# Optimization experiments

Measured on AMD Instinct MI355X. Metric: run time of the kernel, lower is better.

The kernel has to match this reference:

```python
import jax, jax.numpy as jnp
import numpy as np

B, N, IN_DIM, SLOT_DIM, NUM_SLOTS, NUM_ITERS = 64, 4096, 256, 256, 8, 3
LN_EPS = 1e-5


def _ln(x, g, b):
    m = jnp.mean(x, axis=-1, keepdims=True)
    v = jnp.mean(jnp.square(x - m), axis=-1, keepdims=True)
    return (x - m) * jax.lax.rsqrt(v + LN_EPS) * g + b


def setup_inputs() -> dict:
    key = jax.random.key(0)
    ks = jax.random.split(key, 16)
    D, I = SLOT_DIM, IN_DIM
    s = 0.02
    return {
        "inputs": jax.random.normal(ks[0], (B, N, I), jnp.float32),
        "slots_noise": jax.random.normal(ks[1], (B, NUM_SLOTS, D), jnp.float32),
        "slots_mu": jax.random.normal(ks[2], (1, 1, D), jnp.float32),
        "slots_log_sigma": jnp.zeros((1, 1, D), jnp.float32),
        "ln_in_g": jnp.ones((I,), jnp.float32), "ln_in_b": jnp.zeros((I,), jnp.float32),
        "ln_s_g": jnp.ones((D,), jnp.float32), "ln_s_b": jnp.zeros((D,), jnp.float32),
        "ln_m_g": jnp.ones((D,), jnp.float32), "ln_m_b": jnp.zeros((D,), jnp.float32),
        "Wq": jax.random.normal(ks[3], (D, D), jnp.float32) * s,
        "Wk": jax.random.normal(ks[4], (I, D), jnp.float32) * s,
        "Wv": jax.random.normal(ks[5], (I, D), jnp.float32) * s,
        "gru_w_ih": jax.random.normal(ks[6], (3 * D, D), jnp.float32) * s,
        "gru_w_hh": jax.random.normal(ks[7], (3 * D, D), jnp.float32) * s,
        "gru_b_ih": jnp.zeros((3 * D,), jnp.float32),
        "gru_b_hh": jnp.zeros((3 * D,), jnp.float32),
        "mlp_w1": jax.random.normal(ks[8], (D, 4 * D), jnp.float32) * s,
        "mlp_b1": jnp.zeros((4 * D,), jnp.float32),
        "mlp_w2": jax.random.normal(ks[9], (4 * D, D), jnp.float32) * s,
        "mlp_b2": jnp.zeros((D,), jnp.float32),
    }


def reference(inputs, slots_noise, slots_mu, slots_log_sigma, ln_in_g, ln_in_b,
              ln_s_g, ln_s_b, ln_m_g, ln_m_b, Wq, Wk, Wv,
              gru_w_ih, gru_w_hh, gru_b_ih, gru_b_hh,
              mlp_w1, mlp_b1, mlp_w2, mlp_b2):
    D = SLOT_DIM
    # slot init: mu + sigma * noise
    slots = slots_mu + jnp.exp(slots_log_sigma) * slots_noise  # [B, S, D]
    x = _ln(inputs, ln_in_g, ln_in_b)                          # [B, N, I]
    k = x @ Wk                                                 # [B, N, D]
    v = x @ Wv                                                 # [B, N, D]
    scale = 1.0 / jnp.sqrt(jnp.float32(D))
    attn = None
    for _ in range(NUM_ITERS):
        slots_prev = slots
        s_n = _ln(slots, ln_s_g, ln_s_b)
        q = s_n @ Wq                                           # [B, S, D]
        logits = jnp.einsum('bnd,bmd->bnm', k, q) * scale      # [B, N, S]
        attn = jax.nn.softmax(logits, axis=-1)                 # softmax over slots
        attn_nrm = attn / (jnp.sum(attn, axis=1, keepdims=True) + 1e-8)
        updates = jnp.einsum('bnm,bnd->bmd', attn_nrm, v)      # [B, S, D]
        # GRUCell (PyTorch semantics)
        gi = updates @ gru_w_ih.T + gru_b_ih                   # [B, S, 3D]
        gh = slots_prev @ gru_w_hh.T + gru_b_hh
        gi_r, gi_z, gi_n = jnp.split(gi, 3, axis=-1)
        gh_r, gh_z, gh_n = jnp.split(gh, 3, axis=-1)
        r = jax.nn.sigmoid(gi_r + gh_r)
        z = jax.nn.sigmoid(gi_z + gh_z)
        n = jnp.tanh(gi_n + r * gh_n)
        slots = (1.0 - z) * n + z * slots_prev
        # residual MLP
        h = jax.nn.relu(_ln(slots, ln_m_g, ln_m_b) @ mlp_w1 + mlp_b1)
        slots = slots + h @ mlp_w2 + mlp_b2
    return slots, jnp.transpose(attn, (0, 2, 1))
```

## Files before the change

kernel.cpp:

```cpp
#include <hip/hip_runtime.h>


typedef unsigned short u16;
typedef __attribute__((ext_vector_type(8))) short bf16x8;
typedef __attribute__((ext_vector_type(4))) float f32x4;

#define MFMA16(a, b, c) __builtin_amdgcn_mfma_f32_16x16x32_bf16((a), (b), (c), 0, 0, 0)

__device__ __forceinline__ u16 f2bf(float f) {
  union { float f; unsigned u; } v; v.f = f;
  unsigned r = (v.u + 0x7fffu + ((v.u >> 16) & 1u)) >> 16;
  return (u16)r;
}
__device__ __forceinline__ float sigm(float x) { return 1.f / (1.f + __expf(-x)); }
__device__ __forceinline__ float tanh_f(float x) { return 1.f - 2.f / (1.f + __expf(2.f * x)); }

__global__ __launch_bounds__(256) void prep_kernel(
    const float* __restrict__ Wq, const float* __restrict__ Wk, const float* __restrict__ Wv,
    const float* __restrict__ wih, const float* __restrict__ whh,
    const float* __restrict__ w1, const float* __restrict__ w2,
    u16* __restrict__ wkB, u16* __restrict__ wqT, u16* __restrict__ wvT,
    u16* __restrict__ wihB, u16* __restrict__ whhB, u16* __restrict__ w1T, u16* __restrict__ w2T) {
  const int bid = blockIdx.x;
  const int tid = threadIdx.x;
  if (bid < 160) {
    __shared__ float tile[64][65];
    const float* src; u16* dst; int R, C, t;
    if (bid < 16)      { src = Wq; dst = wqT; R = 256;  C = 256;  t = bid; }
    else if (bid < 32) { src = Wv; dst = wvT; R = 256;  C = 256;  t = bid - 16; }
    else if (bid < 96) { src = w1; dst = w1T; R = 1024; C = 256;  t = bid - 32; }
    else               { src = w2; dst = w2T; R = 256;  C = 1024; t = bid - 96; }
    const int tilesJ = C >> 6;
    const int i0 = (t / tilesJ) * 64, j0 = (t % tilesJ) * 64;
    const int c = tid & 63, r0 = tid >> 6;
#pragma unroll
    for (int rr = 0; rr < 16; rr++) {
      int row = rr * 4 + r0;
      tile[row][c] = src[(size_t)(j0 + row) * R + i0 + c];
    }
    __syncthreads();
#pragma unroll
    for (int rr = 0; rr < 16; rr++) {
      int row = rr * 4 + r0;
      dst[(size_t)(i0 + row) * C + j0 + c] = f2bf(tile[c][row]);
    }
  } else {
    int gid = (bid - 160) * 256 + tid;
    for (int i4 = gid; i4 < 114688; i4 += 64 * 256) {
      int i = i4 * 4;
      const float* s; u16* d; int off;
      if (i < 65536) { s = Wk; d = wkB; off = i; }
      else if (i < 262144) { s = wih; d = wihB; off = i - 65536; }
      else { s = whh; d = whhB; off = i - 262144; }
      float4 v = *reinterpret_cast<const float4*>(s + off);
      unsigned lo = (unsigned)f2bf(v.x) | ((unsigned)f2bf(v.y) << 16);
      unsigned hi = (unsigned)f2bf(v.z) | ((unsigned)f2bf(v.w) << 16);
      *reinterpret_cast<uint2*>(d + off) = make_uint2(lo, hi);
    }
  }
}

__device__ __forceinline__ void ln_row16(const float (*src)[264], u16 (*dst)[264],
                                         const float* __restrict__ g, const float* __restrict__ bb,
                                         int wave, int lane) {
  int row = wave;
  if (row < 8) {
    float4 v = *reinterpret_cast<const float4*>(&src[row][lane * 4]);
    float s = v.x + v.y + v.z + v.w;
    float sq = v.x * v.x + v.y * v.y + v.z * v.z + v.w * v.w;
#pragma unroll
    for (int m = 1; m < 64; m <<= 1) { s += __shfl_xor(s, m); sq += __shfl_xor(sq, m); }
    float mu = s * (1.f / 256.f);
    float var = sq * (1.f / 256.f) - mu * mu;
    float rstd = rsqrtf(fmaxf(var, 0.f) + 1e-5f);
    float4 gg = *reinterpret_cast<const float4*>(&g[lane * 4]);
    float4 bv = *reinterpret_cast<const float4*>(&bb[lane * 4]);
    unsigned lo = (unsigned)f2bf((v.x - mu) * rstd * gg.x + bv.x) |
                  ((unsigned)f2bf((v.y - mu) * rstd * gg.y + bv.y) << 16);
    unsigned hi = (unsigned)f2bf((v.z - mu) * rstd * gg.z + bv.z) |
                  ((unsigned)f2bf((v.w - mu) * rstd * gg.w + bv.w) << 16);
    *reinterpret_cast<uint2*>(&dst[row][lane * 4]) = make_uint2(lo, hi);
  } else if (row < 16) {
    *reinterpret_cast<uint2*>(&dst[row][lane * 4]) = make_uint2(0, 0);
  }
}

__global__ __launch_bounds__(1024, 4) void slot_kernel(
    float* __restrict__ slots, u16* __restrict__ qg, float* __restrict__ cd,
    const float* __restrict__ wsY, const float* __restrict__ wsS,
    const u16* __restrict__ wvT, const u16* __restrict__ wihB, const u16* __restrict__ whhB,
    const u16* __restrict__ w1T, const u16* __restrict__ w2T, const u16* __restrict__ wqT,
    const u16* __restrict__ wkB,
    const float* __restrict__ bih, const float* __restrict__ bhh,
    const float* __restrict__ b1v, const float* __restrict__ b2v,
    const float* __restrict__ g_in, const float* __restrict__ b_in,
    const float* __restrict__ g_s, const float* __restrict__ b_s,
    const float* __restrict__ g_m, const float* __restrict__ b_m,
    const float* __restrict__ s_mu, const float* __restrict__ s_ls,
    const float* __restrict__ noise,
    float* __restrict__ d_out, int do_update) {
  __shared__ alignas(16) char pool[58368];
  u16 (*h_lds)[1032] = reinterpret_cast<u16(*)[1032]>(pool);
  u16 (*u_lds)[264] = reinterpret_cast<u16(*)[264]>(pool);
  u16 (*uv_lds)[264] = reinterpret_cast<u16(*)[264]>(pool + 8448);
  u16 (*sb_lds)[264] = reinterpret_cast<u16(*)[264]>(pool + 16896);
  u16 (*m_lds)[264] = reinterpret_cast<u16(*)[264]>(pool + 33024);
  float (*ns_lds)[264] = reinterpret_cast<float(*)[264]>(pool + 41472);
  u16 (*q_lds)[264] = reinterpret_cast<u16(*)[264]>(pool + 41472);
  __shared__ float sS0[16], sS1[16], sInv[16];
  __shared__ float redq[16][4][4][2];

  const int b = blockIdx.x;
  const int tid = threadIdx.x;
  const int lane = tid & 63, wave = tid >> 6;
  const int quad = lane >> 4, col = lane & 15;
  const int i256 = tid & 255, s4 = tid >> 8;
  const f32x4 vzero = {0.f, 0.f, 0.f, 0.f};

  if (do_update) {
    if (tid < 16) {
      float S0 = 0.f, S1 = 0.f;
      if (tid < 8) {
        for (int c = 0; c < 32; c++) {
          S0 += wsS[((b * 32 + c) * 8 + tid) * 2 + 0];
          S1 += wsS[((b * 32 + c) * 8 + tid) * 2 + 1];
        }
      }
      sS0[tid] = S0; sS1[tid] = S1; sInv[tid] = 1.f / (S0 + 1e-8f);
    }
#pragma unroll
    for (int r = 0; r < 4; r++) {
      int s = s4 + r * 4;
      sb_lds[s][i256] = (s < 8) ? f2bf(slots[(size_t)(b * 8 + s) * 256 + i256]) : (u16)0;
    }
    __syncthreads();
    {
      float gv = g_in[i256], bv = b_in[i256];
#pragma unroll
      for (int r = 0; r < 4; r++) {
        int s = s4 + r * 4;
        if (s < 8) {
          float y = 0.f;
#pragma unroll
          for (int c = 0; c < 32; c++) y += wsY[((size_t)((b * 32 + c) * 8 + s)) * 256 + i256];
          u_lds[s][i256] = f2bf((gv * (y - sS1[s]) + bv * sS0[s]) * sInv[s]);
        } else {
          u_lds[s][i256] = 0;
        }
      }
    }
    __syncthreads();
    {
      bf16x8 af[8];
#pragma unroll
      for (int k = 0; k < 8; k++)
        af[k] = *reinterpret_cast<const bf16x8*>(&u_lds[col][k * 32 + quad * 8]);
      int ct = wave;
      f32x4 acc = vzero;
#pragma unroll
      for (int k = 0; k < 8; k++) {
        bf16x8 bf = *reinterpret_cast<const bf16x8*>(wvT + (size_t)(ct * 16 + col) * 256 + k * 32 + quad * 8);
        acc = MFMA16(af[k], bf, acc);
      }
#pragma unroll
      for (int r = 0; r < 4; r++) {
        int s = quad * 4 + r;
        uv_lds[s][ct * 16 + col] = (s < 8) ? f2bf(acc[r]) : (u16)0;
      }
    }
    __syncthreads();
    {
      bf16x8 afu[8], afs[8];
#pragma unroll
      for (int k = 0; k < 8; k++) {
        afu[k] = *reinterpret_cast<const bf16x8*>(&uv_lds[col][k * 32 + quad * 8]);
        afs[k] = *reinterpret_cast<const bf16x8*>(&sb_lds[col][k * 32 + quad * 8]);
      }
      int d = wave * 16 + col;
      f32x4 a_ir = vzero, a_iz = vzero, a_in = vzero, a_hr = vzero, a_hz = vzero, a_hn = vzero;
#pragma unroll
      for (int k = 0; k < 8; k++) {
        int ko = k * 32 + quad * 8;
        a_ir = MFMA16(afu[k], *reinterpret_cast<const bf16x8*>(wihB + (size_t)(d)*256 + ko), a_ir);
        a_iz = MFMA16(afu[k], *reinterpret_cast<const bf16x8*>(wihB + (size_t)(256 + d) * 256 + ko), a_iz);
        a_in = MFMA16(afu[k], *reinterpret_cast<const bf16x8*>(wihB + (size_t)(512 + d) * 256 + ko), a_in);
        a_hr = MFMA16(afs[k], *reinterpret_cast<const bf16x8*>(whhB + (size_t)(d)*256 + ko), a_hr);
        a_hz = MFMA16(afs[k], *reinterpret_cast<const bf16x8*>(whhB + (size_t)(256 + d) * 256 + ko), a_hz);
        a_hn = MFMA16(afs[k], *reinterpret_cast<const bf16x8*>(whhB + (size_t)(512 + d) * 256 + ko), a_hn);
      }
      float bihr = bih[d], bihz = bih[256 + d], bihn = bih[512 + d];
      float bhhr = bhh[d], bhhz = bhh[256 + d], bhhn = bhh[512 + d];
#pragma unroll
      for (int r = 0; r < 4; r++) {
        int s = quad * 4 + r;
        float rg = sigm(a_ir[r] + bihr + a_hr[r] + bhhr);
        float zg = sigm(a_iz[r] + bihz + a_hz[r] + bhhz);
        float ng = tanh_f(a_in[r] + bihn + rg * (a_hn[r] + bhhn));
        float prev = (s < 8) ? slots[(size_t)(b * 8 + s) * 256 + d] : 0.f;
        float ns = (1.f - zg) * ng + zg * prev;
        ns_lds[s][d] = (s < 8) ? ns : 0.f;
      }
    }
    __syncthreads();
    ln_row16(ns_lds, m_lds, g_m, b_m, wave, lane);
    __syncthreads();
    {
      bf16x8 af[8];
#pragma unroll
      for (int k = 0; k < 8; k++)
        af[k] = *reinterpret_cast<const bf16x8*>(&m_lds[col][k * 32 + quad * 8]);
      for (int cc = 0; cc < 4; cc++) {
        int ct = wave * 4 + cc;
        f32x4 acc = vzero;
#pragma unroll
        for (int k = 0; k < 8; k++) {
          bf16x8 bf = *reinterpret_cast<const bf16x8*>(w1T + (size_t)(ct * 16 + col) * 256 + k * 32 + quad * 8);
          acc = MFMA16(af[k], bf, acc);
        }
        float bb = b1v[ct * 16 + col];
#pragma unroll
        for (int r = 0; r < 4; r++) {
          int s = quad * 4 + r;
          float h = fmaxf(acc[r] + bb, 0.f);
          h_lds[s][ct * 16 + col] = (s < 8) ? f2bf(h) : (u16)0;
        }
      }
    }
    __syncthreads();
    {
      int ct = wave;
      f32x4 acc = vzero;
      for (int k = 0; k < 32; k++) {
        bf16x8 af = *reinterpret_cast<const bf16x8*>(&h_lds[col][k * 32 + quad * 8]);
        bf16x8 bf = *reinterpret_cast<const bf16x8*>(w2T + (size_t)(ct * 16 + col) * 1024 + k * 32 + quad * 8);
        acc = MFMA16(af, bf, acc);
      }
      int d = ct * 16 + col;
      float bb = b2v[d];
#pragma unroll
      for (int r = 0; r < 4; r++) {
        int s = quad * 4 + r;
        if (s < 8) {
          float fin = ns_lds[s][d] + acc[r] + bb;
          slots[(size_t)(b * 8 + s) * 256 + d] = fin;
          d_out[(size_t)(b * 8 + s) * 256 + d] = fin;
          ns_lds[s][d] = fin;
        }
      }
    }
    __syncthreads();
  } else {
#pragma unroll
    for (int r = 0; r < 4; r++) {
      int s = s4 + r * 4;
      float v = 0.f;
      if (s < 8) {
        v = s_mu[i256] + __expf(s_ls[i256]) * noise[(size_t)(b * 8 + s) * 256 + i256];
        slots[(size_t)(b * 8 + s) * 256 + i256] = v;
      }
      ns_lds[s][i256] = v;
    }
    __syncthreads();
  }

  ln_row16(ns_lds, m_lds, g_s, b_s, wave, lane);
  __syncthreads();
  {
    bf16x8 af[8];
#pragma unroll
    for (int k = 0; k < 8; k++)
      af[k] = *reinterpret_cast<const bf16x8*>(&m_lds[col][k * 32 + quad * 8]);
    int ct = wave;
    f32x4 acc = vzero;
#pragma unroll
    for (int k = 0; k < 8; k++) {
      bf16x8 bf = *reinterpret_cast<const bf16x8*>(wqT + (size_t)(ct * 16 + col) * 256 + k * 32 + quad * 8);
      acc = MFMA16(af[k], bf, acc);
    }
#pragma unroll
    for (int r = 0; r < 4; r++) {
      int s = quad * 4 + r;
      q_lds[s][ct * 16 + col] = (s < 8) ? f2bf(acc[r]) : (u16)0;
    }
  }
  __syncthreads();
  {
    bf16x8 af[8];
#pragma unroll
    for (int k = 0; k < 8; k++)
      af[k] = *reinterpret_cast<const bf16x8*>(&q_lds[col][k * 32 + quad * 8]);
    float cacc[4] = {0.f, 0.f, 0.f, 0.f}, dacc[4] = {0.f, 0.f, 0.f, 0.f};
    int ct = wave;
    f32x4 acc = vzero;
#pragma unroll
    for (int k = 0; k < 8; k++) {
      bf16x8 bf = *reinterpret_cast<const bf16x8*>(wkB + (size_t)(ct * 16 + col) * 256 + k * 32 + quad * 8);
      acc = MFMA16(af[k], bf, acc);
    }
    int i = ct * 16 + col;
    float gi_ = g_in[i] * 0.0625f, bi_ = b_in[i] * 0.0625f;
#pragma unroll
    for (int r = 0; r < 4; r++) {
      int s = quad * 4 + r;
      float qkv = acc[r];
      float qgv = (s < 8) ? gi_ * qkv : 0.f;
      qg[(size_t)(b * 16 + s) * 256 + i] = f2bf(qgv);
      cacc[r] -= qgv;
      dacc[r] += (s < 8) ? bi_ * qkv : 0.f;
    }
#pragma unroll
    for (int r = 0; r < 4; r++) {
#pragma unroll
      for (int m = 1; m < 16; m <<= 1) {
        cacc[r] += __shfl_xor(cacc[r], m);
        dacc[r] += __shfl_xor(dacc[r], m);
      }
    }
    if (col == 0) {
#pragma unroll
      for (int r = 0; r < 4; r++) {
        redq[wave][quad][r][0] = cacc[r];
        redq[wave][quad][r][1] = dacc[r];
      }
    }
    __syncthreads();
    if (tid < 16) {
      int qd = tid >> 2, r = tid & 3;
      float c = 0.f, dd = 0.f;
      for (int w = 0; w < 16; w++) { c += redq[w][qd][r][0]; dd += redq[w][qd][r][1]; }
      cd[(b * 16 + tid) * 2 + 0] = c;
      cd[(b * 16 + tid) * 2 + 1] = dd;
    }
  }
}

template <int PASS>
__global__ __launch_bounds__(256, 5) void attn_kernel(
    const float* __restrict__ x, u16* __restrict__ xb, float2* __restrict__ stats2,
    const u16* __restrict__ qg, const float* __restrict__ cd,
    float* __restrict__ out, float* __restrict__ wsY, float* __restrict__ wsS) {
  __shared__ alignas(16) u16 x_lds[32][280];
  __shared__ alignas(16) u16 a2s[4][16][40];
  __shared__ float2 stats_lds[32];

  const int chunk = blockIdx.x, b = blockIdx.y;
  const int tid = threadIdx.x;
  const int lane = tid & 63, wave = tid >> 6;
  const int quad = lane >> 4, col = lane & 15;

  const float2 cdv = *reinterpret_cast<const float2*>(cd + (b * 16 + col) * 2);

  f32x4 Yacc[4];
#pragma unroll
  for (int cc = 0; cc < 4; cc++) Yacc[cc] = {0.f, 0.f, 0.f, 0.f};
  float s0a = 0.f, s1a = 0.f;
  float* out_attn = out + 131072;

  for (int g = 0; g < 4; g++) {
    const int nb = chunk * 128 + g * 32;
    __syncthreads();
    if (PASS == 0) {
#pragma unroll
      for (int p = 0; p < 8; p++) {
        const int row = wave * 8 + p;
        float4 v = *reinterpret_cast<const float4*>(x + (size_t)(b * 4096 + nb + row) * 256 + lane * 4);
        unsigned lo = (unsigned)f2bf(v.x) | ((unsigned)f2bf(v.y) << 16);
        unsigned hi = (unsigned)f2bf(v.z) | ((unsigned)f2bf(v.w) << 16);
        *reinterpret_cast<uint2*>(&x_lds[row][lane * 4]) = make_uint2(lo, hi);
        *reinterpret_cast<uint2*>(xb + (size_t)(b * 4096 + nb + row) * 256 + lane * 4) = make_uint2(lo, hi);
      }
    } else {
#pragma unroll
      for (int p = 0; p < 8; p++) {
        const int row = wave * 8 + p;
        *reinterpret_cast<uint2*>(&x_lds[row][lane * 4]) =
            *reinterpret_cast<const uint2*>(xb + (size_t)(b * 4096 + nb + row) * 256 + lane * 4);
      }
      if (tid < 32) stats_lds[tid] = stats2[(size_t)b * 4096 + nb + tid];
    }
    __syncthreads();

    bf16x8 bfrag[8];
#pragma unroll
    for (int k = 0; k < 8; k++)
      bfrag[k] = *reinterpret_cast<const bf16x8*>(qg + (size_t)(b * 16 + col) * 256 + k * 32 + quad * 8);
#pragma unroll
    for (int t = 0; t < 2; t++) {
      bf16x8 af[8];
#pragma unroll
      for (int k = 0; k < 8; k++)
        af[k] = *reinterpret_cast<const bf16x8*>(&x_lds[t * 16 + col][k * 32 + quad * 8]);
      f32x4 acc = {0.f, 0.f, 0.f, 0.f};
#pragma unroll
      for (int k = 0; k < 8; k++) acc = MFMA16(af[k], bfrag[k], acc);

      float rmx[4], rmy[4];
      if (PASS == 0) {
        const short one_bf = (short)0x3F80;
        bf16x8 ones8 = {one_bf, one_bf, one_bf, one_bf, one_bf, one_bf, one_bf, one_bf};
        f32x4 accS = {0.f, 0.f, 0.f, 0.f}, accG = {0.f, 0.f, 0.f, 0.f};
#pragma unroll
        for (int k = 0; k < 8; k++) {
          accS = MFMA16(af[k], ones8, accS);
          accG = MFMA16(af[k], af[k], accG);
        }
#pragma unroll
        for (int r = 0; r < 4; r++) {
          float sq = __shfl(accG[r], (quad << 4) + quad * 4 + r);
          float mu = accS[r] * (1.f / 256.f);
          float var = sq * (1.f / 256.f) - mu * mu;
          float rstd = rsqrtf(fmaxf(var, 0.f) + 1e-5f);
          rmx[r] = rstd; rmy[r] = rstd * mu;
        }
        if (wave == 0 && col == 0) {
#pragma unroll
          for (int r = 0; r < 4; r++)
            stats2[(size_t)b * 4096 + nb + t * 16 + quad * 4 + r] = make_float2(rmx[r], rmy[r]);
        }
      } else {
#pragma unroll
        for (int r = 0; r < 4; r++) {
          float2 rm = stats_lds[t * 16 + quad * 4 + r];
          rmx[r] = rm.x; rmy[r] = rm.y;
        }
      }
      float at[4];
#pragma unroll
      for (int r = 0; r < 4; r++) {
        float lg = rmx[r] * acc[r] + rmy[r] * cdv.x + cdv.y;
        float mx = lg;
        mx = fmaxf(mx, __shfl_xor(mx, 1));
        mx = fmaxf(mx, __shfl_xor(mx, 2));
        mx = fmaxf(mx, __shfl_xor(mx, 4));
        float e = __expf(lg - mx);
        float sm = e;
        sm += __shfl_xor(sm, 1); sm += __shfl_xor(sm, 2); sm += __shfl_xor(sm, 4);
        at[r] = e / sm;
      }
      if (col < 8) {
#pragma unroll
        for (int r = 0; r < 4; r++)
          a2s[wave][col][t * 16 + quad * 4 + r] = f2bf(at[r] * rmx[r]);
        if (wave == 0) {
#pragma unroll
          for (int r = 0; r < 4; r++) {
            out_attn[(size_t)(b * 8 + col) * 4096 + nb + t * 16 + quad * 4 + r] = at[r];
            s0a += at[r];
            s1a += at[r] * rmy[r];
          }
        }
      }
    }
    {
      bf16x8 afa = *reinterpret_cast<const bf16x8*>(&a2s[wave][col][quad * 8]);
#pragma unroll
      for (int cc = 0; cc < 4; cc++) {
        const int ib = (wave * 4 + cc) * 16 + col;
        union { short s[8]; bf16x8 v; } bx;
#pragma unroll
        for (int j = 0; j < 8; j++) bx.s[j] = (short)x_lds[quad * 8 + j][ib];
        Yacc[cc] = MFMA16(afa, bx.v, Yacc[cc]);
      }
    }
  }
  if (quad < 2) {
#pragma unroll
    for (int cc = 0; cc < 4; cc++) {
      int i = (wave * 4 + cc) * 16 + col;
#pragma unroll
      for (int r = 0; r < 4; r++) {
        int s = quad * 4 + r;
        wsY[(size_t)((b * 32 + chunk) * 8 + s) * 256 + i] = Yacc[cc][r];
      }
    }
  }
  s0a += __shfl_xor(s0a, 16); s0a += __shfl_xor(s0a, 32);
  s1a += __shfl_xor(s1a, 16); s1a += __shfl_xor(s1a, 32);
  if (wave == 0 && lane < 8) {
    wsS[((b * 32 + chunk) * 8 + lane) * 2 + 0] = s0a;
    wsS[((b * 32 + chunk) * 8 + lane) * 2 + 1] = s1a;
  }
}

extern "C" void kernel_launch(void* const* d_in, const int* in_sizes, int n_in,
                              void* d_out, int out_size, void* d_ws, size_t ws_size,
                              hipStream_t stream) {
  const float* inputs = (const float*)d_in[0];
  const float* noise = (const float*)d_in[1];
  const float* s_mu = (const float*)d_in[2];
  const float* s_ls = (const float*)d_in[3];
  const float* g_in = (const float*)d_in[4];
  const float* b_in = (const float*)d_in[5];
  const float* g_s = (const float*)d_in[6];
  const float* b_s = (const float*)d_in[7];
  const float* g_m = (const float*)d_in[8];
  const float* b_m = (const float*)d_in[9];
  const float* Wq = (const float*)d_in[10];
  const float* Wk = (const float*)d_in[11];
  const float* Wv = (const float*)d_in[12];
  const float* wih = (const float*)d_in[13];
  const float* whh = (const float*)d_in[14];
  const float* bih = (const float*)d_in[15];
  const float* bhh = (const float*)d_in[16];
  const float* w1 = (const float*)d_in[17];
  const float* b1v = (const float*)d_in[18];
  const float* w2 = (const float*)d_in[19];
  const float* b2v = (const float*)d_in[20];
  float* out = (float*)d_out;

  size_t o = 0;
  auto take = [&](size_t bytes) {
    void* p = (char*)d_ws + o;
    o += (bytes + 255) & ~(size_t)255;
    return p;
  };
  float* slots = (float*)take((size_t)64 * 8 * 256 * 4);
  u16* qg = (u16*)take((size_t)64 * 16 * 256 * 2);
  float* cd = (float*)take((size_t)64 * 16 * 2 * 4);
  float* wsY = (float*)take((size_t)64 * 32 * 8 * 256 * 4);
  float* wsS = (float*)take((size_t)64 * 32 * 8 * 2 * 4);
  u16* wkB = (u16*)take((size_t)65536 * 2);
  u16* wqT = (u16*)take((size_t)65536 * 2);
  u16* wvT = (u16*)take((size_t)65536 * 2);
  u16* wihB = (u16*)take((size_t)196608 * 2);
  u16* whhB = (u16*)take((size_t)196608 * 2);
  u16* w1T = (u16*)take((size_t)262144 * 2);
  u16* w2T = (u16*)take((size_t)262144 * 2);
  u16* xb = (u16*)take((size_t)64 * 4096 * 256 * 2);
  float2* stats2 = (float2*)take((size_t)64 * 4096 * 8);

  prep_kernel<<<224, 256, 0, stream>>>(Wq, Wk, Wv, wih, whh, w1, w2,
                                       wkB, wqT, wvT, wihB, whhB, w1T, w2T);
  slot_kernel<<<64, 1024, 0, stream>>>(slots, qg, cd, wsY, wsS,
                                       wvT, wihB, whhB, w1T, w2T, wqT, wkB,
                                       bih, bhh, b1v, b2v,
                                       g_in, b_in, g_s, b_s, g_m, b_m,
                                       s_mu, s_ls, noise, out, 0);
  for (int it = 0; it < 3; it++) {
    if (it == 0)
      attn_kernel<0><<<dim3(32, 64), 256, 0, stream>>>(inputs, xb, stats2, qg, cd, out, wsY, wsS);
    else
      attn_kernel<1><<<dim3(32, 64), 256, 0, stream>>>(inputs, xb, stats2, qg, cd, out, wsY, wsS);
    slot_kernel<<<64, 1024, 0, stream>>>(slots, qg, cd, wsY, wsS,
                                         wvT, wihB, whhB, w1T, w2T, wqT, wkB,
                                         bih, bhh, b1v, b2v,
                                         g_in, b_in, g_s, b_s, g_m, b_m,
                                         s_mu, s_ls, noise, out, 1);
  }
}
```

Measured before the change: 808.2 us.

## Split input conversion into separate kernel and double-buffer attention tiles

```diff
diff --git a/kernel.cpp b/kernel.cpp
--- a/kernel.cpp
+++ b/kernel.cpp
@@ -14,6 +14,37 @@
 }
 __device__ __forceinline__ float sigm(float x) { return 1.f / (1.f + __expf(-x)); }
 __device__ __forceinline__ float tanh_f(float x) { return 1.f - 2.f / (1.f + __expf(2.f * x)); }
+
+__global__ __launch_bounds__(256, 4) void xcvt_kernel(
+    const float* __restrict__ x, u16* __restrict__ xb, float2* __restrict__ stats2) {
+  const int lane = threadIdx.x & 63;
+  const int gw = blockIdx.x * 4 + (threadIdx.x >> 6);
+#pragma unroll 1
+  for (int it = 0; it < 8; it++) {
+    float4 v[4];
+    int r[4];
+#pragma unroll
+    for (int j = 0; j < 4; j++) {
+      r[j] = (it * 4 + j) * 8192 + gw;
+      v[j] = *reinterpret_cast<const float4*>(x + (size_t)r[j] * 256 + lane * 4);
+    }
+#pragma unroll
+    for (int j = 0; j < 4; j++) {
+      float4 vv = v[j];
+      float s = vv.x + vv.y + vv.z + vv.w;
+      float sq = vv.x * vv.x + vv.y * vv.y + vv.z * vv.z + vv.w * vv.w;
+#pragma unroll
+      for (int m = 1; m < 64; m <<= 1) { s += __shfl_xor(s, m); sq += __shfl_xor(sq, m); }
+      float mu = s * (1.f / 256.f);
+      float var = sq * (1.f / 256.f) - mu * mu;
+      float rstd = rsqrtf(fmaxf(var, 0.f) + 1e-5f);
+      if (lane == 0) stats2[r[j]] = make_float2(rstd, rstd * mu);
+      unsigned lo = (unsigned)f2bf(vv.x) | ((unsigned)f2bf(vv.y) << 16);
+      unsigned hi = (unsigned)f2bf(vv.z) | ((unsigned)f2bf(vv.w) << 16);
+      *reinterpret_cast<uint2*>(xb + (size_t)r[j] * 256 + lane * 4) = make_uint2(lo, hi);
+    }
+  }
+}
 
 __global__ __launch_bounds__(256) void prep_kernel(
     const float* __restrict__ Wq, const float* __restrict__ Wk, const float* __restrict__ Wv,
@@ -334,20 +365,23 @@
   }
 }
 
-template <int PASS>
-__global__ __launch_bounds__(256, 5) void attn_kernel(
-    const float* __restrict__ x, u16* __restrict__ xb, float2* __restrict__ stats2,
+__global__ __launch_bounds__(256, 3) void attn_kernel(
+    const u16* __restrict__ xb, const float2* __restrict__ stats2,
     const u16* __restrict__ qg, const float* __restrict__ cd,
     float* __restrict__ out, float* __restrict__ wsY, float* __restrict__ wsS) {
-  __shared__ alignas(16) u16 x_lds[32][280];
+  __shared__ alignas(16) u16 x_lds[2][32][280];
   __shared__ alignas(16) u16 a2s[4][16][40];
-  __shared__ float2 stats_lds[32];
+  __shared__ float2 stats_lds[2][32];
 
   const int chunk = blockIdx.x, b = blockIdx.y;
   const int tid = threadIdx.x;
   const int lane = tid & 63, wave = tid >> 6;
   const int quad = lane >> 4, col = lane & 15;
 
+  bf16x8 bfrag[8];
+#pragma unroll
+  for (int k = 0; k < 8; k++)
+    bfrag[k] = *reinterpret_cast<const bf16x8*>(qg + (size_t)(b * 16 + col) * 256 + k * 32 + quad * 8);
   const float2 cdv = *reinterpret_cast<const float2*>(cd + (b * 16 + col) * 2);
 
   f32x4 Yacc[4];
@@ -356,78 +390,47 @@
   float s0a = 0.f, s1a = 0.f;
   float* out_attn = out + 131072;
 
+  uint2 pf[8];
+  float2 pfs;
+  {
+    const int nb0 = chunk * 128;
+#pragma unroll
+    for (int p = 0; p < 8; p++)
+      pf[p] = *reinterpret_cast<const uint2*>(xb + (size_t)(b * 4096 + nb0 + wave * 8 + p) * 256 + lane * 4);
+    if (tid < 32) pfs = stats2[(size_t)b * 4096 + nb0 + tid];
+#pragma unroll
+    for (int p = 0; p < 8; p++)
+      *reinterpret_cast<uint2*>(&x_lds[0][wave * 8 + p][lane * 4]) = pf[p];
+    if (tid < 32) stats_lds[0][tid] = pfs;
+  }
+
   for (int g = 0; g < 4; g++) {
+    const int cur = g & 1;
     const int nb = chunk * 128 + g * 32;
     __syncthreads();
-    if (PASS == 0) {
-#pragma unroll
-      for (int p = 0; p < 8; p++) {
-        const int row = wave * 8 + p;
-        float4 v = *reinterpret_cast<const float4*>(x + (size_t)(b * 4096 + nb + row) * 256 + lane * 4);
-        unsigned lo = (unsigned)f2bf(v.x) | ((unsigned)f2bf(v.y) << 16);
-        unsigned hi = (unsigned)f2bf(v.z) | ((unsigned)f2bf(v.w) << 16);
-        *reinterpret_cast<uint2*>(&x_lds[row][lane * 4]) = make_uint2(lo, hi);
-        *reinterpret_cast<uint2*>(xb + (size_t)(b * 4096 + nb + row) * 256 + lane * 4) = make_uint2(lo, hi);
-      }
-    } else {
-#pragma unroll
-      for (int p = 0; p < 8; p++) {
-        const int row = wave * 8 + p;
-        *reinterpret_cast<uint2*>(&x_lds[row][lane * 4]) =
-            *reinterpret_cast<const uint2*>(xb + (size_t)(b * 4096 + nb + row) * 256 + lane * 4);
-      }
-      if (tid < 32) stats_lds[tid] = stats2[(size_t)b * 4096 + nb + tid];
-    }
-    __syncthreads();
-
-    bf16x8 bfrag[8];
-#pragma unroll
-    for (int k = 0; k < 8; k++)
-      bfrag[k] = *reinterpret_cast<const bf16x8*>(qg + (size_t)(b * 16 + col) * 256 + k * 32 + quad * 8);
+    if (g < 3) {
+      const int nbn = nb + 32;
+#pragma unroll
+      for (int p = 0; p < 8; p++)
+        pf[p] = *reinterpret_cast<const uint2*>(xb + (size_t)(b * 4096 + nbn + wave * 8 + p) * 256 + lane * 4);
+      if (tid < 32) pfs = stats2[(size_t)b * 4096 + nbn + tid];
+    }
 #pragma unroll
     for (int t = 0; t < 2; t++) {
       bf16x8 af[8];
 #pragma unroll
       for (int k = 0; k < 8; k++)
-        af[k] = *reinterpret_cast<const bf16x8*>(&x_lds[t * 16 + col][k * 32 + quad * 8]);
+        af[k] = *reinterpret_cast<const bf16x8*>(&x_lds[cur][t * 16 + col][k * 32 + quad * 8]);
       f32x4 acc = {0.f, 0.f, 0.f, 0.f};
 #pragma unroll
       for (int k = 0; k < 8; k++) acc = MFMA16(af[k], bfrag[k], acc);
 
-      float rmx[4], rmy[4];
-      if (PASS == 0) {
-        const short one_bf = (short)0x3F80;
-        bf16x8 ones8 = {one_bf, one_bf, one_bf, one_bf, one_bf, one_bf, one_bf, one_bf};
-        f32x4 accS = {0.f, 0.f, 0.f, 0.f}, accG = {0.f, 0.f, 0.f, 0.f};
-#pragma unroll
-        for (int k = 0; k < 8; k++) {
-          accS = MFMA16(af[k], ones8, accS);
-          accG = MFMA16(af[k], af[k], accG);
-        }
-#pragma unroll
-        for (int r = 0; r < 4; r++) {
-          float sq = __shfl(accG[r], (quad << 4) + quad * 4 + r);
-          float mu = accS[r] * (1.f / 256.f);
-          float var = sq * (1.f / 256.f) - mu * mu;
-          float rstd = rsqrtf(fmaxf(var, 0.f) + 1e-5f);
-          rmx[r] = rstd; rmy[r] = rstd * mu;
-        }
-        if (wave == 0 && col == 0) {
-#pragma unroll
-          for (int r = 0; r < 4; r++)
-            stats2[(size_t)b * 4096 + nb + t * 16 + quad * 4 + r] = make_float2(rmx[r], rmy[r]);
-        }
-      } else {
-#pragma unroll
-        for (int r = 0; r < 4; r++) {
-          float2 rm = stats_lds[t * 16 + quad * 4 + r];
-          rmx[r] = rm.x; rmy[r] = rm.y;
-        }
-      }
-      float at[4];
-#pragma unroll
-      for (int r = 0; r < 4; r++) {
-        float lg = rmx[r] * acc[r] + rmy[r] * cdv.x + cdv.y;
+      float at[4], rmx[4], rmy[4];
+#pragma unroll
+      for (int r = 0; r < 4; r++) {
+        float2 rm = stats_lds[cur][t * 16 + quad * 4 + r];
+        rmx[r] = rm.x; rmy[r] = rm.y;
+        float lg = rm.x * acc[r] + rm.y * cdv.x + cdv.y;
         float mx = lg;
         mx = fmaxf(mx, __shfl_xor(mx, 1));
         mx = fmaxf(mx, __shfl_xor(mx, 2));
@@ -458,9 +461,15 @@
         const int ib = (wave * 4 + cc) * 16 + col;
         union { short s[8]; bf16x8 v; } bx;
 #pragma unroll
-        for (int j = 0; j < 8; j++) bx.s[j] = (short)x_lds[quad * 8 + j][ib];
+        for (int j = 0; j < 8; j++) bx.s[j] = (short)x_lds[cur][quad * 8 + j][ib];
         Yacc[cc] = MFMA16(afa, bx.v, Yacc[cc]);
       }
+    }
+    if (g < 3) {
+#pragma unroll
+      for (int p = 0; p < 8; p++)
+        *reinterpret_cast<uint2*>(&x_lds[cur ^ 1][wave * 8 + p][lane * 4]) = pf[p];
+      if (tid < 32) stats_lds[cur ^ 1][tid] = pfs;
     }
   }
   if (quad < 2) {
@@ -531,16 +540,14 @@
 
   prep_kernel<<<224, 256, 0, stream>>>(Wq, Wk, Wv, wih, whh, w1, w2,
                                        wkB, wqT, wvT, wihB, whhB, w1T, w2T);
+  xcvt_kernel<<<2048, 256, 0, stream>>>(inputs, xb, stats2);
   slot_kernel<<<64, 1024, 0, stream>>>(slots, qg, cd, wsY, wsS,
                                        wvT, wihB, whhB, w1T, w2T, wqT, wkB,
                                        bih, bhh, b1v, b2v,
                                        g_in, b_in, g_s, b_s, g_m, b_m,
                                        s_mu, s_ls, noise, out, 0);
   for (int it = 0; it < 3; it++) {
-    if (it == 0)
-      attn_kernel<0><<<dim3(32, 64), 256, 0, stream>>>(inputs, xb, stats2, qg, cd, out, wsY, wsS);
-    else
-      attn_kernel<1><<<dim3(32, 64), 256, 0, stream>>>(inputs, xb, stats2, qg, cd, out, wsY, wsS);
+    attn_kernel<<<dim3(32, 64), 256, 0, stream>>>(xb, stats2, qg, cd, out, wsY, wsS);
     slot_kernel<<<64, 1024, 0, stream>>>(slots, qg, cd, wsY, wsS,
                                          wvT, wihB, whhB, w1T, w2T, wqT, wkB,
                                          bih, bhh, b1v, b2v,
```

Result: faster. 778.8 us (-3.6%).
